# Kernel optimization log

Hardware: AMD Instinct MI355X
Metric: run time of the kernel (lower is better)

Reference implementation:

```python
import jax, jax.numpy as jnp
import numpy as np
import math
from jax import lax

VOCAB = 32000
D = 128          # embedding_dim
S = 512          # seq_len == input_channels
B = 8
HID = 512        # hidden_size
NBUCK = 32       # n_buckets
NHYP = 5         # log2(n_buckets)
ENCODERS = 2
OUT = 6
EPS = 1e-5


def _positional_encoding(max_len, d):
    pos = np.arange(max_len, dtype=np.float32)[:, None]
    div = np.exp(np.arange(0, d, 2, dtype=np.float32) * (-math.log(10000.0) / d))
    pe = np.zeros((max_len, d), dtype=np.float32)
    pe[:, 0::2] = np.sin(pos * div)
    pe[:, 1::2] = np.cos(pos * div)
    return jnp.asarray(pe)


def setup_inputs() -> dict:
    key = jax.random.key(0)
    ks = jax.random.split(key, 10)
    emb = jax.random.normal(ks[0], (VOCAB, D), jnp.float32)
    emb = emb.at[VOCAB - 1].set(0.0)  # padding_idx row is zero in torch
    sc = 0.05
    return {
        "inputs": jax.random.randint(ks[1], (B, S), 0, VOCAB - 1),
        "emb": emb,
        # Faithful quirk: pe is indexed by x.size(0)=batch, so only pe[:B] is used.
        "pe": _positional_encoding(B, D),               # [B, D]
        "hyperplanes": jax.random.normal(ks[2], (D + 1, NHYP), jnp.float32),
        "Wq": jax.random.normal(ks[3], (D, D), jnp.float32) * sc,
        "bq": jnp.zeros((D,), jnp.float32),
        "Wv": jax.random.normal(ks[4], (D, D), jnp.float32) * sc,
        "bv": jnp.zeros((D,), jnp.float32),
        "ln_g": jnp.ones((D,), jnp.float32),
        "ln_b": jnp.zeros((D,), jnp.float32),
        "W1": jax.random.normal(ks[5], (D, HID), jnp.float32) * sc,
        "b1": jnp.zeros((HID,), jnp.float32),
        "W2": jax.random.normal(ks[6], (HID, D), jnp.float32) * sc,
        "b2": jnp.zeros((D,), jnp.float32),
        "Wm": jax.random.normal(ks[7], (S * D, OUT), jnp.float32) * 0.01,
        "bm": jnp.zeros((OUT,), jnp.float32),
    }


def _layernorm(x, g, b):
    mu = jnp.mean(x, axis=-1, keepdims=True)
    var = jnp.mean(jnp.square(x - mu), axis=-1, keepdims=True)
    return (x - mu) * lax.rsqrt(var + EPS) * g + b


def _lsh_attention(x, Wq, bq, Wv, bv, hyperplanes):
    q = x @ Wq + bq                                      # [B,S,D]
    v = x @ Wv + bv                                      # [B,S,D]
    # LSH bucket ids from q (hard threshold -> no grad through buckets)
    qh = jnp.concatenate([q, jnp.ones(q.shape[:-1] + (1,), q.dtype)], axis=-1)
    proj = jnp.einsum('bse,en->bsn', qh, hyperplanes)    # [B,S,NHYP]
    bits = (proj >= 0).astype(jnp.float32)
    pow2 = 2.0 ** jnp.arange(NHYP, dtype=jnp.float32)
    buckets = jnp.einsum('bsn,n->bs', bits, pow2).astype(jnp.int32)  # [B,S]
    scale = 1.0 / math.sqrt(D)

    def step(acc, i):
        # Faithful quirk: masked_fill zeros tokens IN bucket i (inverted mask).
        keep = (buckets != i)[..., None]                 # [B,S,1]
        qb = jnp.where(keep, q, 0.0)
        vb = jnp.where(keep, v, 0.0)
        att = jax.nn.softmax(jnp.einsum('bsd,btd->bst', qb, qb) * scale, axis=-1)
        return acc + jnp.einsum('bst,btd->bsd', att, vb), None

    out, _ = lax.scan(step, jnp.zeros_like(x), jnp.arange(NBUCK))
    return out


def reference(inputs, emb, pe, hyperplanes, Wq, bq, Wv, bv, ln_g, ln_b,
              W1, b1, W2, b2, Wm, bm):
    x = emb[inputs]                                      # [B,S,D]
    x = x + pe[:, None, :]                               # broadcast over seq (faithful quirk)
    for _ in range(ENCODERS):
        a = _lsh_attention(x, Wq, bq, Wv, bv, hyperplanes)
        x = _layernorm(a, ln_g, ln_b)
        x = (jax.nn.relu(x @ W1 + b1) @ W2 + b2) + x     # fc residual (dropout=eval)
        x = _layernorm(x, ln_g, ln_b)
    x = x.reshape(x.shape[0], -1)                        # [B, S*D]
    return x @ Wm + bm                                   # [B, OUT]
```

## Files before the change

kernel.cpp:

```cpp
#include <hip/hip_runtime.h>
#include <hip/hip_bf16.h>

#define BB   8
#define SS   512
#define DD   128
#define HH   512
#define NBK  32


__global__ void k_embed(const int* __restrict__ idx, const float* __restrict__ emb,
                        const float* __restrict__ pe, float* __restrict__ x) {
    int b = blockIdx.x;
    int t = b * 16384 + blockIdx.y * 256 + threadIdx.x;
    int tok = t >> 5, d4 = (t & 31) * 4;
    float4 ev = *(const float4*)&emb[(size_t)idx[tok] * DD + d4];
    float4 pv = *(const float4*)&pe[b * DD + d4];
    ev.x += pv.x; ev.y += pv.y; ev.z += pv.z; ev.w += pv.w;
    *(float4*)&x[(size_t)tok * DD + d4] = ev;
}

__global__ __launch_bounds__(256) void k_qvb(const float* __restrict__ x,
        const float* __restrict__ Wq, const float* __restrict__ bq,
        const float* __restrict__ Wv, const float* __restrict__ bv,
        const float* __restrict__ hyp,
        float* __restrict__ q, float* __restrict__ v, float* __restrict__ qT,
        int* __restrict__ bucket) {
    int rb = blockIdx.x * 32 + blockIdx.y;
    __shared__ __align__(16) float xs[16][132];
    __shared__ float qts[128][17];
    int tid = threadIdx.x;
    #pragma unroll
    for (int it = 0; it < 2; ++it) {
        int lin = tid + 256 * it;
        int r = lin >> 5, kq = (lin & 31) * 4;
        *(float4*)&xs[r][kq] = *(const float4*)&x[(size_t)(rb * 16 + r) * DD + kq];
    }
    __syncthreads();
    int tx = tid & 63;
    int ty = tid >> 6;
    float2 aq[4], av[4];
    #pragma unroll
    for (int i = 0; i < 4; ++i) { aq[i] = make_float2(0.f, 0.f); av[i] = make_float2(0.f, 0.f); }
    for (int g = 0; g < 32; ++g) {
        int kb = g * 4;
        float4 a0 = *(const float4*)&xs[ty * 4 + 0][kb];
        float4 a1 = *(const float4*)&xs[ty * 4 + 1][kb];
        float4 a2 = *(const float4*)&xs[ty * 4 + 2][kb];
        float4 a3 = *(const float4*)&xs[ty * 4 + 3][kb];
        #pragma unroll
        for (int j = 0; j < 4; ++j) {
            float2 wq = *(const float2*)&Wq[(size_t)(kb + j) * DD + tx * 2];
            float2 wv = *(const float2*)&Wv[(size_t)(kb + j) * DD + tx * 2];
            float c0 = (j == 0) ? a0.x : (j == 1) ? a0.y : (j == 2) ? a0.z : a0.w;
            float c1 = (j == 0) ? a1.x : (j == 1) ? a1.y : (j == 2) ? a1.z : a1.w;
            float c2 = (j == 0) ? a2.x : (j == 1) ? a2.y : (j == 2) ? a2.z : a2.w;
            float c3 = (j == 0) ? a3.x : (j == 1) ? a3.y : (j == 2) ? a3.z : a3.w;
            aq[0].x += c0 * wq.x; aq[0].y += c0 * wq.y; av[0].x += c0 * wv.x; av[0].y += c0 * wv.y;
            aq[1].x += c1 * wq.x; aq[1].y += c1 * wq.y; av[1].x += c1 * wv.x; av[1].y += c1 * wv.y;
            aq[2].x += c2 * wq.x; aq[2].y += c2 * wq.y; av[2].x += c2 * wv.x; av[2].y += c2 * wv.y;
            aq[3].x += c3 * wq.x; aq[3].y += c3 * wq.y; av[3].x += c3 * wv.x; av[3].y += c3 * wv.y;
        }
    }
    float2 bqv = *(const float2*)&bq[tx * 2];
    float2 bvv = *(const float2*)&bv[tx * 2];
    float2 oq[4], ov[4];
    #pragma unroll
    for (int i = 0; i < 4; ++i) {
        oq[i] = make_float2(aq[i].x + bqv.x, aq[i].y + bqv.y);
        ov[i] = make_float2(av[i].x + bvv.x, av[i].y + bvv.y);
        int row = rb * 16 + ty * 4 + i;
        *(float2*)&q[(size_t)row * DD + tx * 2] = oq[i];
        *(float2*)&v[(size_t)row * DD + tx * 2] = ov[i];
        qts[2 * tx][ty * 4 + i]     = oq[i].x;
        qts[2 * tx + 1][ty * 4 + i] = oq[i].y;
    }
    float h0[5], h1[5];
    #pragma unroll
    for (int h = 0; h < 5; ++h) {
        h0[h] = hyp[(2 * tx) * 5 + h];
        h1[h] = hyp[(2 * tx + 1) * 5 + h];
    }
    float pr[4][5];
    #pragma unroll
    for (int r = 0; r < 4; ++r)
        #pragma unroll
        for (int h = 0; h < 5; ++h)
            pr[r][h] = oq[r].x * h0[h] + oq[r].y * h1[h];
    #pragma unroll
    for (int o = 1; o < 64; o <<= 1)
        #pragma unroll
        for (int r = 0; r < 4; ++r)
            #pragma unroll
            for (int h = 0; h < 5; ++h)
                pr[r][h] += __shfl_xor(pr[r][h], o, 64);
    if (tx == 0) {
        #pragma unroll
        for (int r = 0; r < 4; ++r) {
            int bb = 0;
            #pragma unroll
            for (int h = 0; h < 5; ++h)
                if (pr[r][h] + hyp[128 * 5 + h] >= 0.f) bb |= (1 << h);
            bucket[rb * 16 + ty * 4 + r] = bb;
        }
    }
    __syncthreads();
    {
        int b  = blockIdx.x;
        int t0 = blockIdx.y * 16;
        int k  = tid >> 1, o = (tid & 1) * 8;
        float4 v0 = make_float4(qts[k][o], qts[k][o + 1], qts[k][o + 2], qts[k][o + 3]);
        float4 v1 = make_float4(qts[k][o + 4], qts[k][o + 5], qts[k][o + 6], qts[k][o + 7]);
        size_t base = ((size_t)b * DD + k) * SS + t0 + o;
        *(float4*)&qT[base]     = v0;
        *(float4*)&qT[base + 4] = v1;
    }
}

__global__ __launch_bounds__(256) void k_vb(const float* __restrict__ v,
        const int* __restrict__ bucket, float* __restrict__ Vb,
        int* __restrict__ cnt) {
    int b  = blockIdx.x;
    int bk = blockIdx.y;
    int tid = threadIdx.x;
    __shared__ int bkt_sh[512];
    __shared__ float red[128];
    bkt_sh[tid]       = bucket[b * SS + tid];
    bkt_sh[tid + 256] = bucket[b * SS + tid + 256];
    __syncthreads();
    int d = tid & 127, half = tid >> 7;
    const float* vbp = v + (size_t)b * SS * DD + d;
    float acc = 0.f;
    #pragma unroll 8
    for (int i = 0; i < 256; ++i) {
        int tok = half * 256 + i;
        float val = vbp[(size_t)tok * DD];
        acc += (bkt_sh[tok] == bk) ? val : 0.f;
    }
    if (half == 1) red[d] = acc;
    __syncthreads();
    if (half == 0)
        Vb[(size_t)((b << 5) + bk) * DD + d] = acc + red[d];
    if (tid < 64) {
        int c = 0;
        #pragma unroll
        for (int i = 0; i < 8; ++i) c += (bkt_sh[tid * 8 + i] == bk) ? 1 : 0;
        #pragma unroll
        for (int o = 1; o < 64; o <<= 1) c += __shfl_xor(c, o, 64);
        if (tid == 0) cnt[(b << 5) + bk] = c;
    }
}

__global__ __launch_bounds__(512) void k_enc(const float* __restrict__ qT,
        const float* __restrict__ q, const float* __restrict__ v,
        const int* __restrict__ bucket, const int* __restrict__ cnt,
        const float* __restrict__ Vb,
        const float* __restrict__ g, const float* __restrict__ lb,
        const float* __restrict__ W1, const float* __restrict__ b1,
        const float* __restrict__ W2, const float* __restrict__ b2,
        float* __restrict__ x) {
    int bz = blockIdx.x, s0 = blockIdx.y * 16;
    int tid = threadIdx.x;
    __shared__ __align__(16) float qs[16][132];
    __shared__ __align__(16) float cs[16][528];
    __shared__ __align__(16) float osh[16][132];
    __shared__ int   bkt[512];
    __shared__ float Wsh[16][32];
    __shared__ float rsh[16][32];
    __shared__ float Zsh[16], Rsh[16], Msh[16];
    __shared__ float cntf[32];
    __shared__ int   bssh[16];
    {
        int r = tid >> 5, kq = (tid & 31) * 4;
        *(float4*)&qs[r][kq] = *(const float4*)&q[(size_t)(bz * SS + s0 + r) * DD + kq];
    }
    bkt[tid] = bucket[bz * SS + tid];
    if (tid < 32) cntf[tid] = (float)cnt[(bz << 5) + tid];
    if (tid < 16) bssh[tid] = bucket[bz * SS + s0 + tid];
    Wsh[tid >> 5][tid & 31] = 0.f;
    __syncthreads();
    const float scale = 0.088388347648318447f;
    {
        int kh   = tid >> 8;
        int rg   = (tid >> 7) & 1;
        int slot = tid & 127;
        float4 acc[8];
        #pragma unroll
        for (int i = 0; i < 8; ++i) acc[i] = make_float4(0.f, 0.f, 0.f, 0.f);
        const float* qtb = qT + (size_t)bz * DD * SS + (size_t)kh * 64 * SS + slot * 4;
        for (int gg = 0; gg < 16; ++gg) {
            int kb = kh * 64 + gg * 4;
            float4 a[8];
            #pragma unroll
            for (int i = 0; i < 8; ++i) a[i] = *(const float4*)&qs[rg * 8 + i][kb];
            #pragma unroll
            for (int j = 0; j < 4; ++j) {
                float4 b4 = *(const float4*)&qtb[(size_t)(gg * 4 + j) * SS];
                #pragma unroll
                for (int i = 0; i < 8; ++i) {
                    float c = (j == 0) ? a[i].x : (j == 1) ? a[i].y : (j == 2) ? a[i].z : a[i].w;
                    acc[i].x += c * b4.x; acc[i].y += c * b4.y;
                    acc[i].z += c * b4.z; acc[i].w += c * b4.w;
                }
            }
        }
        if (kh == 1) {
            #pragma unroll
            for (int i = 0; i < 8; ++i)
                *(float4*)&cs[rg * 8 + i][slot * 4] = acc[i];
        }
        __syncthreads();
        if (kh == 0) {
            #pragma unroll
            for (int i = 0; i < 8; ++i) {
                float4 p = *(const float4*)&cs[rg * 8 + i][slot * 4];
                p.x = (p.x + acc[i].x) * scale;
                p.y = (p.y + acc[i].y) * scale;
                p.z = (p.z + acc[i].z) * scale;
                p.w = (p.w + acc[i].w) * scale;
                *(float4*)&cs[rg * 8 + i][slot * 4] = p;
            }
        }
        __syncthreads();
    }
    int row = tid >> 5, l = tid & 31;
    {
        float m = 0.f;
        #pragma unroll
        for (int i = 0; i < 16; ++i) m = fmaxf(m, cs[row][l + 32 * i]);
        #pragma unroll
        for (int o = 1; o < 32; o <<= 1) m = fmaxf(m, __shfl_xor(m, o, 32));
        if (l == 0) Msh[row] = m;
    }
    __syncthreads();
    {
        float Ms = Msh[row];
        #pragma unroll
        for (int i = 0; i < 16; ++i) {
            int c = l + 32 * i;
            float ev = __expf(cs[row][c] - Ms);
            cs[row][c] = ev;
            atomicAdd(&Wsh[row][bkt[c]], ev);
        }
    }
    __syncthreads();
    if (tid < 16) {
        float z = 0.f;
        #pragma unroll
        for (int i = 0; i < NBK; ++i) z += Wsh[tid][i];
        Zsh[tid] = z;
    }
    __syncthreads();
    rsh[row][l] = 1.0f / (Zsh[row] - Wsh[row][l] + cntf[l] * __expf(-Msh[row]));
    __syncthreads();
    if (tid < 16) {
        int bs = bssh[tid];
        float R = 0.f;
        #pragma unroll
        for (int i = 0; i < NBK; ++i) R += (i == bs) ? 0.f : rsh[tid][i];
        Rsh[tid] = R;
    }
    __syncthreads();
    {
        float R = Rsh[row];
        int bs = bssh[row];
        #pragma unroll
        for (int i = 0; i < 16; ++i) {
            int c = l + 32 * i;
            int bc = bkt[c];
            float rsel = (bc == bs) ? 0.f : rsh[row][bc];
            cs[row][c] *= (R - rsel);
        }
    }
    __syncthreads();
    {
        int kh = tid >> 7;
        int rg = (tid >> 5) & 3;
        int cp = tid & 31;
        float4 acc[4];
        #pragma unroll
        for (int i = 0; i < 4; ++i) acc[i] = make_float4(0.f, 0.f, 0.f, 0.f);
        const float* vb_base = v + (size_t)bz * SS * DD + cp * 4;
        for (int gg = 0; gg < 32; ++gg) {
            int kb = kh * 128 + gg * 4;
            float4 a[4];
            #pragma unroll
            for (int i = 0; i < 4; ++i) a[i] = *(const float4*)&cs[rg * 4 + i][kb];
            #pragma unroll
            for (int j = 0; j < 4; ++j) {
                float4 vj = *(const float4*)&vb_base[(size_t)(kb + j) * DD];
                #pragma unroll
                for (int i = 0; i < 4; ++i) {
                    float c = (j == 0) ? a[i].x : (j == 1) ? a[i].y : (j == 2) ? a[i].z : a[i].w;
                    acc[i].x += c * vj.x; acc[i].y += c * vj.y;
                    acc[i].z += c * vj.z; acc[i].w += c * vj.w;
                }
            }
        }
        if (kh == 3) {
            #pragma unroll
            for (int i = 0; i < 4; ++i)
                *(float4*)&osh[rg * 4 + i][cp * 4] = acc[i];
        }
        __syncthreads();
        #pragma unroll
        for (int p = 2; p >= 1; --p) {
            if (kh == p) {
                #pragma unroll
                for (int i = 0; i < 4; ++i) {
                    float4 o = *(const float4*)&osh[rg * 4 + i][cp * 4];
                    o.x += acc[i].x; o.y += acc[i].y; o.z += acc[i].z; o.w += acc[i].w;
                    *(float4*)&osh[rg * 4 + i][cp * 4] = o;
                }
            }
            __syncthreads();
        }
        if (kh == 0) {
            float4 vs = make_float4(0.f, 0.f, 0.f, 0.f);
            #pragma unroll
            for (int i = 0; i < NBK; ++i) {
                float4 t = *(const float4*)&Vb[(size_t)((bz << 5) + i) * DD + cp * 4];
                vs.x += t.x; vs.y += t.y; vs.z += t.z; vs.w += t.w;
            }
            const float inv512 = 1.0f / 512.0f;
            #pragma unroll
            for (int i = 0; i < 4; ++i) {
                int r = rg * 4 + i;
                int bs = bssh[r];
                float4 vb4 = *(const float4*)&Vb[(size_t)((bz << 5) + bs) * DD + cp * 4];
                float4 p = *(const float4*)&osh[r][cp * 4];
                p.x += acc[i].x + (vs.x - vb4.x) * inv512;
                p.y += acc[i].y + (vs.y - vb4.y) * inv512;
                p.z += acc[i].z + (vs.z - vb4.z) * inv512;
                p.w += acc[i].w + (vs.w - vb4.w) * inv512;
                *(float4*)&osh[r][cp * 4] = p;
            }
        }
        __syncthreads();
    }
    {
        float4 val = *(const float4*)&osh[row][l * 4];
        float s = val.x + val.y + val.z + val.w;
        float ss = val.x * val.x + val.y * val.y + val.z * val.z + val.w * val.w;
        #pragma unroll
        for (int o = 1; o < 32; o <<= 1) {
            s  += __shfl_xor(s, o, 32);
            ss += __shfl_xor(ss, o, 32);
        }
        float mean = s * (1.f / 128.f);
        float var = ss * (1.f / 128.f) - mean * mean;
        float rstd = rsqrtf(var + 1e-5f);
        float4 gv = *(const float4*)&g[l * 4];
        float4 bv = *(const float4*)&lb[l * 4];
        float4 out;
        out.x = (val.x - mean) * rstd * gv.x + bv.x;
        out.y = (val.y - mean) * rstd * gv.y + bv.y;
        out.z = (val.z - mean) * rstd * gv.z + bv.z;
        out.w = (val.w - mean) * rstd * gv.w + bv.w;
        *(float4*)&qs[row][l * 4] = out;
    }
    __syncthreads();
    {
        int kh   = tid >> 8;
        int rg   = (tid >> 7) & 1;
        int slot = tid & 127;
        float4 acc[8];
        #pragma unroll
        for (int i = 0; i < 8; ++i) acc[i] = make_float4(0.f, 0.f, 0.f, 0.f);
        for (int gg = 0; gg < 16; ++gg) {
            int kb = kh * 64 + gg * 4;
            float4 a[8];
            #pragma unroll
            for (int i = 0; i < 8; ++i) a[i] = *(const float4*)&qs[rg * 8 + i][kb];
            #pragma unroll
            for (int j = 0; j < 4; ++j) {
                float4 w = *(const float4*)&W1[(size_t)(kb + j) * HH + slot * 4];
                #pragma unroll
                for (int i = 0; i < 8; ++i) {
                    float c = (j == 0) ? a[i].x : (j == 1) ? a[i].y : (j == 2) ? a[i].z : a[i].w;
                    acc[i].x += c * w.x; acc[i].y += c * w.y;
                    acc[i].z += c * w.z; acc[i].w += c * w.w;
                }
            }
        }
        if (kh == 1) {
            #pragma unroll
            for (int i = 0; i < 8; ++i)
                *(float4*)&cs[rg * 8 + i][slot * 4] = acc[i];
        }
        __syncthreads();
        if (kh == 0) {
            float4 bi = *(const float4*)&b1[slot * 4];
            #pragma unroll
            for (int i = 0; i < 8; ++i) {
                float4 p = *(const float4*)&cs[rg * 8 + i][slot * 4];
                p.x = fmaxf(p.x + acc[i].x + bi.x, 0.f);
                p.y = fmaxf(p.y + acc[i].y + bi.y, 0.f);
                p.z = fmaxf(p.z + acc[i].z + bi.z, 0.f);
                p.w = fmaxf(p.w + acc[i].w + bi.w, 0.f);
                *(float4*)&cs[rg * 8 + i][slot * 4] = p;
            }
        }
        __syncthreads();
    }
    {
        int kh = tid >> 7;
        int rg = (tid >> 5) & 3;
        int cp = tid & 31;
        float4 acc[4];
        #pragma unroll
        for (int i = 0; i < 4; ++i) acc[i] = make_float4(0.f, 0.f, 0.f, 0.f);
        for (int gg = 0; gg < 32; ++gg) {
            int kb = kh * 128 + gg * 4;
            float4 a[4];
            #pragma unroll
            for (int i = 0; i < 4; ++i) a[i] = *(const float4*)&cs[rg * 4 + i][kb];
            #pragma unroll
            for (int j = 0; j < 4; ++j) {
                float4 w = *(const float4*)&W2[(size_t)(kb + j) * DD + cp * 4];
                #pragma unroll
                for (int i = 0; i < 4; ++i) {
                    float c = (j == 0) ? a[i].x : (j == 1) ? a[i].y : (j == 2) ? a[i].z : a[i].w;
                    acc[i].x += c * w.x; acc[i].y += c * w.y;
                    acc[i].z += c * w.z; acc[i].w += c * w.w;
                }
            }
        }
        if (kh == 3) {
            #pragma unroll
            for (int i = 0; i < 4; ++i)
                *(float4*)&osh[rg * 4 + i][cp * 4] = acc[i];
        }
        __syncthreads();
        #pragma unroll
        for (int p = 2; p >= 1; --p) {
            if (kh == p) {
                #pragma unroll
                for (int i = 0; i < 4; ++i) {
                    float4 o = *(const float4*)&osh[rg * 4 + i][cp * 4];
                    o.x += acc[i].x; o.y += acc[i].y; o.z += acc[i].z; o.w += acc[i].w;
                    *(float4*)&osh[rg * 4 + i][cp * 4] = o;
                }
            }
            __syncthreads();
        }
        if (kh == 0) {
            float4 bi = *(const float4*)&b2[cp * 4];
            #pragma unroll
            for (int i = 0; i < 4; ++i) {
                int r = rg * 4 + i;
                float4 res = *(const float4*)&qs[r][cp * 4];
                float4 p = *(const float4*)&osh[r][cp * 4];
                p.x += acc[i].x + bi.x + res.x;
                p.y += acc[i].y + bi.y + res.y;
                p.z += acc[i].z + bi.z + res.z;
                p.w += acc[i].w + bi.w + res.w;
                *(float4*)&osh[r][cp * 4] = p;
            }
        }
        __syncthreads();
    }
    {
        float4 val = *(const float4*)&osh[row][l * 4];
        float s = val.x + val.y + val.z + val.w;
        float ss = val.x * val.x + val.y * val.y + val.z * val.z + val.w * val.w;
        #pragma unroll
        for (int o = 1; o < 32; o <<= 1) {
            s  += __shfl_xor(s, o, 32);
            ss += __shfl_xor(ss, o, 32);
        }
        float mean = s * (1.f / 128.f);
        float var = ss * (1.f / 128.f) - mean * mean;
        float rstd = rsqrtf(var + 1e-5f);
        float4 gv = *(const float4*)&g[l * 4];
        float4 bv = *(const float4*)&lb[l * 4];
        float4 out;
        out.x = (val.x - mean) * rstd * gv.x + bv.x;
        out.y = (val.y - mean) * rstd * gv.y + bv.y;
        out.z = (val.z - mean) * rstd * gv.z + bv.z;
        out.w = (val.w - mean) * rstd * gv.w + bv.w;
        *(float4*)&x[(size_t)(bz * SS + s0 + row) * DD + l * 4] = out;
    }
}

__global__ __launch_bounds__(256) void k_final(const float* __restrict__ x,
        const float* __restrict__ Wm, const float* __restrict__ bm,
        float* __restrict__ out) {
    int b = blockIdx.x, chunk = blockIdx.y;
    int tid = threadIdx.x;
    const float* xr = x + (size_t)b * 65536 + chunk * 2048;
    const float* wr = Wm + (size_t)(chunk * 2048) * 6;
    float p[6] = {0.f, 0.f, 0.f, 0.f, 0.f, 0.f};
    #pragma unroll
    for (int it = 0; it < 2; ++it) {
        int j = (tid + 256 * it) * 4;
        float4 xv = *(const float4*)&xr[j];
        const float* w = wr + (size_t)j * 6;
        float4 w0 = *(const float4*)&w[0];
        float4 w1 = *(const float4*)&w[4];
        float4 w2 = *(const float4*)&w[8];
        float4 w3 = *(const float4*)&w[12];
        float4 w4 = *(const float4*)&w[16];
        float4 w5 = *(const float4*)&w[20];
        p[0] += xv.x * w0.x + xv.y * w1.z + xv.z * w3.x + xv.w * w4.z;
        p[1] += xv.x * w0.y + xv.y * w1.w + xv.z * w3.y + xv.w * w4.w;
        p[2] += xv.x * w0.z + xv.y * w2.x + xv.z * w3.z + xv.w * w5.x;
        p[3] += xv.x * w0.w + xv.y * w2.y + xv.z * w3.w + xv.w * w5.y;
        p[4] += xv.x * w1.x + xv.y * w2.z + xv.z * w4.x + xv.w * w5.z;
        p[5] += xv.x * w1.y + xv.y * w2.w + xv.z * w4.y + xv.w * w5.w;
    }
    #pragma unroll
    for (int o = 0; o < 6; ++o)
        #pragma unroll
        for (int off = 1; off < 64; off <<= 1)
            p[o] += __shfl_xor(p[o], off, 64);
    __shared__ float red[4][6];
    int wv = tid >> 6;
    if ((tid & 63) == 0)
        #pragma unroll
        for (int o = 0; o < 6; ++o) red[wv][o] = p[o];
    __syncthreads();
    if (tid < 6) {
        float sv = red[0][tid] + red[1][tid] + red[2][tid] + red[3][tid];
        if (chunk == 0) sv += bm[tid];
        atomicAdd(&out[b * 6 + tid], sv);
    }
}

extern "C" void kernel_launch(void* const* d_in, const int* in_sizes, int n_in,
                              void* d_out, int out_size, void* d_ws, size_t ws_size,
                              hipStream_t stream) {
    const int*   inputs = (const int*)  d_in[0];
    const float* emb    = (const float*)d_in[1];
    const float* pe     = (const float*)d_in[2];
    const float* hyp    = (const float*)d_in[3];
    const float* Wq     = (const float*)d_in[4];
    const float* bq     = (const float*)d_in[5];
    const float* Wv     = (const float*)d_in[6];
    const float* bv     = (const float*)d_in[7];
    const float* ln_g   = (const float*)d_in[8];
    const float* ln_b   = (const float*)d_in[9];
    const float* W1     = (const float*)d_in[10];
    const float* b1     = (const float*)d_in[11];
    const float* W2     = (const float*)d_in[12];
    const float* b2     = (const float*)d_in[13];
    const float* Wm     = (const float*)d_in[14];
    const float* bm     = (const float*)d_in[15];

    float* F = (float*)d_ws;
    float* x     = F + 0;
    float* q     = F + 524288;
    float* v     = F + 1048576;
    float* qT    = F + 1572864;
    float* Vb    = F + 2097152;
    int*   cnt   = (int*)(F + 2129920);
    int*   bucket= (int*)(F + 2130176);

    hipMemsetAsync(d_out, 0, (size_t)out_size * 4, stream);
    k_embed<<<dim3(8, 64), 256, 0, stream>>>(inputs, emb, pe, x);

    for (int enc = 0; enc < 2; ++enc) {
        k_qvb<<<dim3(8, 32), 256, 0, stream>>>(x, Wq, bq, Wv, bv, hyp, q, v, qT, bucket);
        k_vb<<<dim3(8, 32), 256, 0, stream>>>(v, bucket, Vb, cnt);
        k_enc<<<dim3(8, 32), 512, 0, stream>>>(qT, q, v, bucket, cnt, Vb,
                                               ln_g, ln_b, W1, b1, W2, b2, x);
    }
    k_final<<<dim3(8, 32), 256, 0, stream>>>(x, Wm, bm, (float*)d_out);
}
```

Before: 251.7 us.

## Fuse embedding gather into QV kernel and parallelize split-K reduction in shared memory

Removes the separate embedding kernel by gathering embedding rows plus positional encoding directly into the first encoder's QV projection load. Also replaces the serialized three-step split-K reduction (several syncthreads with one wavegroup active at a time) with per-slice shared buffers that are summed in the layernorm step. This saves a launch, a global round trip for x, and barriers, at the cost of four times the osh shared memory, which may reduce occupancy.

```diff
diff --git a/kernel.cpp b/kernel.cpp
--- a/kernel.cpp
+++ b/kernel.cpp
@@ -8,18 +8,9 @@
 #define NBK  32
 
 
-__global__ void k_embed(const int* __restrict__ idx, const float* __restrict__ emb,
-                        const float* __restrict__ pe, float* __restrict__ x) {
-    int b = blockIdx.x;
-    int t = b * 16384 + blockIdx.y * 256 + threadIdx.x;
-    int tok = t >> 5, d4 = (t & 31) * 4;
-    float4 ev = *(const float4*)&emb[(size_t)idx[tok] * DD + d4];
-    float4 pv = *(const float4*)&pe[b * DD + d4];
-    ev.x += pv.x; ev.y += pv.y; ev.z += pv.z; ev.w += pv.w;
-    *(float4*)&x[(size_t)tok * DD + d4] = ev;
-}
-
 __global__ __launch_bounds__(256) void k_qvb(const float* __restrict__ x,
+        const int* __restrict__ idx, const float* __restrict__ emb,
+        const float* __restrict__ pe, int use_emb,
         const float* __restrict__ Wq, const float* __restrict__ bq,
         const float* __restrict__ Wv, const float* __restrict__ bv,
         const float* __restrict__ hyp,
@@ -33,7 +24,17 @@
     for (int it = 0; it < 2; ++it) {
         int lin = tid + 256 * it;
         int r = lin >> 5, kq = (lin & 31) * 4;
-        *(float4*)&xs[r][kq] = *(const float4*)&x[(size_t)(rb * 16 + r) * DD + kq];
+        int tokg = rb * 16 + r;
+        float4 xv;
+        if (use_emb) {
+            int e = idx[tokg];
+            xv = *(const float4*)&emb[(size_t)e * DD + kq];
+            float4 pv = *(const float4*)&pe[blockIdx.x * DD + kq];
+            xv.x += pv.x; xv.y += pv.y; xv.z += pv.z; xv.w += pv.w;
+        } else {
+            xv = *(const float4*)&x[(size_t)tokg * DD + kq];
+        }
+        *(float4*)&xs[r][kq] = xv;
     }
     __syncthreads();
     int tx = tid & 63;
@@ -162,7 +163,7 @@
     int tid = threadIdx.x;
     __shared__ __align__(16) float qs[16][132];
     __shared__ __align__(16) float cs[16][528];
-    __shared__ __align__(16) float osh[16][132];
+    __shared__ __align__(16) float osh[4][16][132];
     __shared__ int   bkt[512];
     __shared__ float Wsh[16][32];
     __shared__ float rsh[16][32];
@@ -296,24 +297,6 @@
                 }
             }
         }
-        if (kh == 3) {
-            #pragma unroll
-            for (int i = 0; i < 4; ++i)
-                *(float4*)&osh[rg * 4 + i][cp * 4] = acc[i];
-        }
-        __syncthreads();
-        #pragma unroll
-        for (int p = 2; p >= 1; --p) {
-            if (kh == p) {
-                #pragma unroll
-                for (int i = 0; i < 4; ++i) {
-                    float4 o = *(const float4*)&osh[rg * 4 + i][cp * 4];
-                    o.x += acc[i].x; o.y += acc[i].y; o.z += acc[i].z; o.w += acc[i].w;
-                    *(float4*)&osh[rg * 4 + i][cp * 4] = o;
-                }
-            }
-            __syncthreads();
-        }
         if (kh == 0) {
             float4 vs = make_float4(0.f, 0.f, 0.f, 0.f);
             #pragma unroll
@@ -327,18 +310,27 @@
                 int r = rg * 4 + i;
                 int bs = bssh[r];
                 float4 vb4 = *(const float4*)&Vb[(size_t)((bz << 5) + bs) * DD + cp * 4];
-                float4 p = *(const float4*)&osh[r][cp * 4];
-                p.x += acc[i].x + (vs.x - vb4.x) * inv512;
-                p.y += acc[i].y + (vs.y - vb4.y) * inv512;
-                p.z += acc[i].z + (vs.z - vb4.z) * inv512;
-                p.w += acc[i].w + (vs.w - vb4.w) * inv512;
-                *(float4*)&osh[r][cp * 4] = p;
-            }
-        }
+                acc[i].x += (vs.x - vb4.x) * inv512;
+                acc[i].y += (vs.y - vb4.y) * inv512;
+                acc[i].z += (vs.z - vb4.z) * inv512;
+                acc[i].w += (vs.w - vb4.w) * inv512;
+            }
+        }
+        #pragma unroll
+        for (int i = 0; i < 4; ++i)
+            *(float4*)&osh[kh][rg * 4 + i][cp * 4] = acc[i];
         __syncthreads();
     }
     {
-        float4 val = *(const float4*)&osh[row][l * 4];
+        float4 p0 = *(const float4*)&osh[0][row][l * 4];
+        float4 p1 = *(const float4*)&osh[1][row][l * 4];
+        float4 p2 = *(const float4*)&osh[2][row][l * 4];
+        float4 p3 = *(const float4*)&osh[3][row][l * 4];
+        float4 val;
+        val.x = p0.x + p1.x + p2.x + p3.x;
+        val.y = p0.y + p1.y + p2.y + p3.y;
+        val.z = p0.z + p1.z + p2.z + p3.z;
+        val.w = p0.w + p1.w + p2.w + p3.w;
         float s = val.x + val.y + val.z + val.w;
         float ss = val.x * val.x + val.y * val.y + val.z * val.z + val.w * val.w;
         #pragma unroll
@@ -425,42 +417,33 @@
                 }
             }
         }
-        if (kh == 3) {
-            #pragma unroll
-            for (int i = 0; i < 4; ++i)
-                *(float4*)&osh[rg * 4 + i][cp * 4] = acc[i];
-        }
-        __syncthreads();
-        #pragma unroll
-        for (int p = 2; p >= 1; --p) {
-            if (kh == p) {
-                #pragma unroll
-                for (int i = 0; i < 4; ++i) {
-                    float4 o = *(const float4*)&osh[rg * 4 + i][cp * 4];
-                    o.x += acc[i].x; o.y += acc[i].y; o.z += acc[i].z; o.w += acc[i].w;
-                    *(float4*)&osh[rg * 4 + i][cp * 4] = o;
-                }
-            }
-            __syncthreads();
-        }
         if (kh == 0) {
             float4 bi = *(const float4*)&b2[cp * 4];
             #pragma unroll
             for (int i = 0; i < 4; ++i) {
                 int r = rg * 4 + i;
                 float4 res = *(const float4*)&qs[r][cp * 4];
-                float4 p = *(const float4*)&osh[r][cp * 4];
-                p.x += acc[i].x + bi.x + res.x;
-                p.y += acc[i].y + bi.y + res.y;
-                p.z += acc[i].z + bi.z + res.z;
-                p.w += acc[i].w + bi.w + res.w;
-                *(float4*)&osh[r][cp * 4] = p;
-            }
-        }
+                acc[i].x += bi.x + res.x;
+                acc[i].y += bi.y + res.y;
+                acc[i].z += bi.z + res.z;
+                acc[i].w += bi.w + res.w;
+            }
+        }
+        #pragma unroll
+        for (int i = 0; i < 4; ++i)
+            *(float4*)&osh[kh][rg * 4 + i][cp * 4] = acc[i];
         __syncthreads();
     }
     {
-        float4 val = *(const float4*)&osh[row][l * 4];
+        float4 p0 = *(const float4*)&osh[0][row][l * 4];
+        float4 p1 = *(const float4*)&osh[1][row][l * 4];
+        float4 p2 = *(const float4*)&osh[2][row][l * 4];
+        float4 p3 = *(const float4*)&osh[3][row][l * 4];
+        float4 val;
+        val.x = p0.x + p1.x + p2.x + p3.x;
+        val.y = p0.y + p1.y + p2.y + p3.y;
+        val.z = p0.z + p1.z + p2.z + p3.z;
+        val.w = p0.w + p1.w + p2.w + p3.w;
         float s = val.x + val.y + val.z + val.w;
         float ss = val.x * val.x + val.y * val.y + val.z * val.z + val.w * val.w;
         #pragma unroll
@@ -556,10 +539,10 @@
     int*   bucket= (int*)(F + 2130176);
 
     hipMemsetAsync(d_out, 0, (size_t)out_size * 4, stream);
-    k_embed<<<dim3(8, 64), 256, 0, stream>>>(inputs, emb, pe, x);
 
     for (int enc = 0; enc < 2; ++enc) {
-        k_qvb<<<dim3(8, 32), 256, 0, stream>>>(x, Wq, bq, Wv, bv, hyp, q, v, qT, bucket);
+        k_qvb<<<dim3(8, 32), 256, 0, stream>>>(x, inputs, emb, pe, enc == 0 ? 1 : 0,
+                                               Wq, bq, Wv, bv, hyp, q, v, qT, bucket);
         k_vb<<<dim3(8, 32), 256, 0, stream>>>(v, bucket, Vb, cnt);
         k_enc<<<dim3(8, 32), 512, 0, stream>>>(qT, q, v, bucket, cnt, Vb,
                                                ln_g, ln_b, W1, b1, W2, b2, x);
```

Measured after the change: 246.4 us. 2.1% less time.
